# Optimization experiments

Measured on AMD Instinct MI355X. Metric: run time of the kernel, lower is better.

## Reference

```python
import jax, jax.numpy as jnp
import numpy as np
from jax import lax

B, T, D, H = 64, 1024, 256, 512


def setup_inputs() -> dict:
    key = jax.random.key(0)
    k1, k2, k3, k4, k5 = jax.random.split(key, 5)
    s = 1.0 / np.sqrt(H)
    return {
        "x": jax.random.normal(k1, (B, T, D), dtype=jnp.float32),
        "W_ih": jax.random.uniform(k2, (4 * H, D), minval=-s, maxval=s, dtype=jnp.float32),
        "W_hh": jax.random.uniform(k3, (4 * H, H), minval=-s, maxval=s, dtype=jnp.float32),
        "b_ih": jax.random.uniform(k4, (4 * H,), minval=-s, maxval=s, dtype=jnp.float32),
        "b_hh": jax.random.uniform(k5, (4 * H,), minval=-s, maxval=s, dtype=jnp.float32),
    }


def reference(x, W_ih, W_hh, b_ih, b_hh):
    # x: [B, T, D] -> time-major [T, B, D]
    xT = jnp.swapaxes(x, 0, 1)
    b, h_dim = x.shape[0], W_hh.shape[1]
    # Precompute input projections for all timesteps: [T, B, 4H]
    x_proj = jnp.einsum("tbd,gd->tbg", xT, W_ih) + b_ih + b_hh

    def step(carry, xg):
        h, c = carry
        gates = xg + h @ W_hh.T  # [B, 4H]
        i, f, g, o = jnp.split(gates, 4, axis=-1)
        c = jax.nn.sigmoid(f) * c + jax.nn.sigmoid(i) * jnp.tanh(g)
        h = jax.nn.sigmoid(o) * jnp.tanh(c)
        return (h, c), jax.nn.sigmoid(h)

    h0 = jnp.zeros((b, h_dim), dtype=x.dtype)
    c0 = jnp.zeros((b, h_dim), dtype=x.dtype)
    _, outs = lax.scan(step, (h0, c0), x_proj)  # outs: [T, B, H]
    # torch.cat along dim 0 over timesteps -> [T*B, H]
    return outs.reshape(-1, h_dim)
```

## Files before the change

### kernel.cpp

```cpp
#include <hip/hip_runtime.h>
#include <stdint.h>

#define T_STEPS 1024
#define BATCH   64
#define DIN     256
#define HDIM    512
#define G4      2048
#define NGRP    8
#define GWG     32
#define GB      8
#define NBUF    16

#define OFF_XCNT  0
#define OFF_ARR   1024
#define OFF_BIAS  8192
#define OFF_WHH   16384
#define OFF_WIH   (OFF_WHH + G4*HDIM*2)
#define OFF_H     (OFF_WIH + G4*DIN*2)

typedef __attribute__((ext_vector_type(8))) short bf16x8;
typedef __attribute__((ext_vector_type(4))) float f32x4;

__device__ __forceinline__ unsigned short f2bf(float f) {
  union { float f; unsigned u; } v; v.f = f;
  unsigned r = v.u + 0x7FFF + ((v.u >> 16) & 1);
  return (unsigned short)(r >> 16);
}
__device__ __forceinline__ float sigm(float x)   { return 1.0f / (1.0f + __expf(-x)); }
__device__ __forceinline__ float tanh_f(float x) { return 2.0f / (1.0f + __expf(-2.0f * x)) - 1.0f; }

__global__ void k_init(unsigned char* ws) {
  int tid = blockIdx.x * blockDim.x + threadIdx.x;
  unsigned* w32 = (unsigned*)ws;
  for (int i = tid; i < 8192 / 4; i += gridDim.x * blockDim.x) w32[i] = 0;
}

__global__ void k_pack(const float* __restrict__ W_ih, const float* __restrict__ W_hh,
                       const float* __restrict__ b_ih, const float* __restrict__ b_hh,
                       unsigned char* ws) {
  unsigned short* whh = (unsigned short*)(ws + OFF_WHH);
  unsigned short* wih = (unsigned short*)(ws + OFF_WIH);
  float* bias = (float*)(ws + OFF_BIAS);
  int tid = blockIdx.x * blockDim.x + threadIdx.x;
  int np = gridDim.x * blockDim.x;
  for (int i = tid; i < G4 * HDIM; i += np) whh[i] = f2bf(W_hh[i]);
  for (int i = tid; i < G4 * DIN;  i += np) wih[i] = f2bf(W_ih[i]);
  for (int i = tid; i < G4;        i += np) bias[i] = b_ih[i] + b_hh[i];
}

__device__ __forceinline__ void stage_x(const float* __restrict__ x, unsigned short* A_s,
                                        int g, int m, int c, int tstep) {
  const float* xb = x + ((size_t)(g * GB + m) * 1024 + tstep) * 256 + c * 8;
  float4 f0 = *(const float4*)(xb);
  float4 f1 = *(const float4*)(xb + 4);
  union { bf16x8 v; unsigned short s[8]; } u;
  u.s[0] = f2bf(f0.x); u.s[1] = f2bf(f0.y); u.s[2] = f2bf(f0.z); u.s[3] = f2bf(f0.w);
  u.s[4] = f2bf(f1.x); u.s[5] = f2bf(f1.y); u.s[6] = f2bf(f1.z); u.s[7] = f2bf(f1.w);
  *(bf16x8*)(A_s + m * 776 + 512 + c * 8) = u.v;
}

__global__ __launch_bounds__(256, 1) void k_lstm(unsigned char* ws,
                                                 const float* __restrict__ x,
                                                 float* __restrict__ out) {
  __shared__ __attribute__((aligned(16))) unsigned short A_s[16 * 776];
  __shared__ __attribute__((aligned(16))) float glp[4 * 16 * 64];
  __shared__ int s_rank;

  const int tid = threadIdx.x;

  unsigned xcc;
  asm("s_getreg_b32 %0, hwreg(HW_REG_XCC_ID)" : "=s"(xcc));
  xcc &= 7;
  unsigned* xcnt = (unsigned*)(ws + OFF_XCNT);
  if (tid == 0)
    s_rank = (int)__hip_atomic_fetch_add(&xcnt[xcc], 1u, __ATOMIC_RELAXED, __HIP_MEMORY_SCOPE_AGENT);
  __syncthreads();
  const int rank = s_rank;
  if (rank >= GWG) return;

  const int g  = (int)xcc;
  const int jt = rank;

  const unsigned short* whh_g = (const unsigned short*)(ws + OFF_WHH);
  const unsigned short* wih_g = (const unsigned short*)(ws + OFF_WIH);
  const float*          bias_g = (const float*)(ws + OFF_BIAS);
  unsigned short*       hring = (unsigned short*)(ws + OFF_H) + (size_t)g * (NBUF * GB * HDIM);
  unsigned*             arr   = (unsigned*)(ws + OFF_ARR + g * 256);

  const int lane = tid & 63, wave = tid >> 6;
  const int arow = lane & 15;
  const int kg   = (lane >> 4) * 8;
  const int sm   = tid >> 5, sc = tid & 31;

  bf16x8 bq[24];
  {
    #pragma unroll
    for (int u = 0; u < 6; ++u)
      #pragma unroll
      for (int nt = 0; nt < 4; ++nt) {
        int grow = nt * 512 + jt * 16 + (lane & 15);
        const unsigned short* src;
        if (u < 4) src = whh_g + (size_t)grow * 512 + (wave * 4 + u) * 32 + kg;
        else       src = wih_g + (size_t)grow * 256 + (wave * 2 + (u - 4)) * 32 + kg;
        bq[u * 4 + nt] = *(const bf16x8*)src;
      }
  }

  {
    unsigned* a32 = (unsigned*)A_s;
    for (int i = tid; i < 16 * 776 / 2; i += 256) a32[i] = 0;
  }

  float biasr[4];
  float c_reg = 0.f;
  const int ub = tid >> 4, jl = tid & 15;
  if (tid < 128) {
    #pragma unroll
    for (int gt = 0; gt < 4; ++gt)
      biasr[gt] = bias_g[gt * 512 + jt * 16 + jl];
  }

  __syncthreads();

  stage_x(x, A_s, g, sm, sc, 0);
  __syncthreads();
  f32x4 accX[4];
  {
    #pragma unroll
    for (int nt = 0; nt < 4; ++nt) accX[nt] = (f32x4){0.f, 0.f, 0.f, 0.f};
    #pragma unroll
    for (int j = 0; j < 2; ++j) {
      int xk = wave * 2 + j;
      bf16x8 a = *(const bf16x8*)(A_s + arow * 776 + 512 + xk * 32 + kg);
      #pragma unroll
      for (int nt = 0; nt < 4; ++nt)
        accX[nt] = __builtin_amdgcn_mfma_f32_16x16x32_bf16(a, bq[(4 + j) * 4 + nt], accX[nt], 0, 0, 0);
    }
  }
  __syncthreads();
  stage_x(x, A_s, g, sm, sc, 1);
  __syncthreads();

  for (int t = 0; t < T_STEPS; ++t) {
    f32x4 acc[4];
    #pragma unroll
    for (int nt = 0; nt < 4; ++nt) acc[nt] = accX[nt];
    #pragma unroll
    for (int u = 0; u < 4; ++u) {
      int kk = wave * 4 + u;
      bf16x8 a = *(const bf16x8*)(A_s + arow * 776 + kk * 32 + kg);
      #pragma unroll
      for (int nt = 0; nt < 4; ++nt)
        acc[nt] = __builtin_amdgcn_mfma_f32_16x16x32_bf16(a, bq[u * 4 + nt], acc[nt], 0, 0, 0);
    }
    #pragma unroll
    for (int nt = 0; nt < 4; ++nt)
      #pragma unroll
      for (int r = 0; r < 4; ++r) {
        int m = (lane >> 4) * 4 + r;
        glp[wave * 1024 + m * 64 + nt * 16 + (lane & 15)] = acc[nt][r];
      }
    __syncthreads();

    float hv = 0.f;
    if (tid < 128) {
      float gs[4];
      #pragma unroll
      for (int gt = 0; gt < 4; ++gt)
        gs[gt] = glp[ub * 64 + gt * 16 + jl]
               + glp[1024 + ub * 64 + gt * 16 + jl]
               + glp[2048 + ub * 64 + gt * 16 + jl]
               + glp[3072 + ub * 64 + gt * 16 + jl] + biasr[gt];
      float cv = sigm(gs[1]) * c_reg + sigm(gs[0]) * tanh_f(gs[2]);
      c_reg = cv;
      hv = sigm(gs[3]) * tanh_f(cv);
      if (t + 1 < T_STEPS) {
        unsigned short* hd = hring + (size_t)((t + 1) & (NBUF - 1)) * (GB * HDIM);
        hd[ub * HDIM + jt * 16 + jl] = f2bf(hv);
        asm volatile("s_waitcnt vmcnt(0)" ::: "memory");
        if (lane == 0)
          __hip_atomic_fetch_add(&arr[wave * 32], 1u,
                                 __ATOMIC_RELAXED, __HIP_MEMORY_SCOPE_WORKGROUP);
      }
      out[((size_t)t * 64 + g * GB + ub) * 512 + jt * 16 + jl] = sigm(hv);
    }

    if (t + 1 < T_STEPS) {
      #pragma unroll
      for (int nt = 0; nt < 4; ++nt) accX[nt] = (f32x4){0.f, 0.f, 0.f, 0.f};
      #pragma unroll
      for (int j = 0; j < 2; ++j) {
        int xk = wave * 2 + j;
        bf16x8 a = *(const bf16x8*)(A_s + arow * 776 + 512 + xk * 32 + kg);
        #pragma unroll
        for (int nt = 0; nt < 4; ++nt)
          accX[nt] = __builtin_amdgcn_mfma_f32_16x16x32_bf16(a, bq[(4 + j) * 4 + nt], accX[nt], 0, 0, 0);
      }
      if (tid == 192) {
        const unsigned target = 32u * (unsigned)(t + 1);
        for (;;) {
          unsigned v0 = __hip_atomic_fetch_or(&arr[0], 0x80000000u,
                                              __ATOMIC_RELAXED, __HIP_MEMORY_SCOPE_WORKGROUP);
          unsigned v1 = __hip_atomic_fetch_or(&arr[32], 0x80000000u,
                                              __ATOMIC_RELAXED, __HIP_MEMORY_SCOPE_WORKGROUP);
          if ((v0 & 0x7FFFFFFFu) >= target && (v1 & 0x7FFFFFFFu) >= target) break;
        }
      }
      __syncthreads();
      {
        const unsigned short* hs = hring + (size_t)((t + 1) & (NBUF - 1)) * (GB * HDIM)
                                 + sm * HDIM + sc * 16;
        bf16x8 h0 = *(const bf16x8*)(hs);
        bf16x8 h1 = *(const bf16x8*)(hs + 8);
        *(bf16x8*)(A_s + sm * 776 + sc * 16)     = h0;
        *(bf16x8*)(A_s + sm * 776 + sc * 16 + 8) = h1;
        if (t + 2 < T_STEPS) stage_x(x, A_s, g, sm, sc, t + 2);
      }
      __syncthreads();
    }
  }
}

extern "C" void kernel_launch(void* const* d_in, const int* in_sizes, int n_in,
                              void* d_out, int out_size, void* d_ws, size_t ws_size,
                              hipStream_t stream) {
  const float* x    = (const float*)d_in[0];
  const float* W_ih = (const float*)d_in[1];
  const float* W_hh = (const float*)d_in[2];
  const float* b_ih = (const float*)d_in[3];
  const float* b_hh = (const float*)d_in[4];
  float* out = (float*)d_out;
  unsigned char* ws = (unsigned char*)d_ws;

  hipLaunchKernelGGL(k_init, dim3(8),    dim3(256), 0, stream, ws);
  hipLaunchKernelGGL(k_pack, dim3(1024), dim3(256), 0, stream, W_ih, W_hh, b_ih, b_hh, ws);
  hipLaunchKernelGGL(k_lstm, dim3(512),  dim3(256), 0, stream, ws, x, out);
}
```

Baseline: 2.849 ms.

## Double workgroup to 8 waves, split gate columns per wave, stage weights in LDS

Workgroups grow from 4 to 8 waves. Each wave now owns one 16-column gate tile, and the K dimension is split unevenly: four waves cover the last four h-chunks plus the whole x projection, the other four cover the first twelve h-chunks. Weights move from per-lane registers into LDS, and the cross-wave reduction shrinks from four partials to two. The arrival counter becomes a single word polled with s_sleep. The intent is shorter per-step MFMA chains on the serial critical path, paid for with LDS reads of the weights every step and a larger block.

```diff
diff --git a/kernel.cpp b/kernel.cpp
--- a/kernel.cpp
+++ b/kernel.cpp
@@ -10,6 +10,7 @@
 #define GWG     32
 #define GB      8
 #define NBUF    16
+#define BLOCK   512
 
 #define OFF_XCNT  0
 #define OFF_ARR   1024
@@ -59,11 +60,13 @@
   *(bf16x8*)(A_s + m * 776 + 512 + c * 8) = u.v;
 }
 
-__global__ __launch_bounds__(256, 1) void k_lstm(unsigned char* ws,
-                                                 const float* __restrict__ x,
-                                                 float* __restrict__ out) {
+__global__ __launch_bounds__(BLOCK, 1) void k_lstm(unsigned char* ws,
+                                                   const float* __restrict__ x,
+                                                   float* __restrict__ out) {
   __shared__ __attribute__((aligned(16))) unsigned short A_s[16 * 776];
-  __shared__ __attribute__((aligned(16))) float glp[4 * 16 * 64];
+  __shared__ __attribute__((aligned(16))) unsigned short Whh_s[64 * 520];
+  __shared__ __attribute__((aligned(16))) unsigned short Wih_s[64 * 264];
+  __shared__ __attribute__((aligned(16))) float glp[2 * 16 * 64];
   __shared__ int s_rank;
 
   const int tid = threadIdx.x;
@@ -85,30 +88,31 @@
   const unsigned short* wih_g = (const unsigned short*)(ws + OFF_WIH);
   const float*          bias_g = (const float*)(ws + OFF_BIAS);
   unsigned short*       hring = (unsigned short*)(ws + OFF_H) + (size_t)g * (NBUF * GB * HDIM);
-  unsigned*             arr   = (unsigned*)(ws + OFF_ARR + g * 256);
-
-  const int lane = tid & 63, wave = tid >> 6;
+  unsigned*             arr   = (unsigned*)(ws + OFF_ARR + g * 128);
+
+  const int lane = tid & 63, w = tid >> 6;
+  const int ns   = w & 3;
+  const int whigh = (w < 4);
   const int arow = lane & 15;
   const int kg   = (lane >> 4) * 8;
-  const int sm   = tid >> 5, sc = tid & 31;
-
-  bf16x8 bq[24];
+  const int rl   = ns * 16 + (lane & 15);
+
   {
-    #pragma unroll
-    for (int u = 0; u < 6; ++u)
-      #pragma unroll
-      for (int nt = 0; nt < 4; ++nt) {
-        int grow = nt * 512 + jt * 16 + (lane & 15);
-        const unsigned short* src;
-        if (u < 4) src = whh_g + (size_t)grow * 512 + (wave * 4 + u) * 32 + kg;
-        else       src = wih_g + (size_t)grow * 256 + (wave * 2 + (u - 4)) * 32 + kg;
-        bq[u * 4 + nt] = *(const bf16x8*)src;
-      }
+    int rl0 = tid >> 3, part = tid & 7;
+    int grow = (rl0 >> 4) * 512 + jt * 16 + (rl0 & 15);
+    const unsigned short* src = whh_g + (size_t)grow * 512 + part * 64;
+    unsigned short* dst = Whh_s + rl0 * 520 + part * 64;
+    #pragma unroll
+    for (int i = 0; i < 8; ++i) *(bf16x8*)(dst + i * 8) = *(const bf16x8*)(src + i * 8);
+    const unsigned short* src2 = wih_g + (size_t)grow * 256 + part * 32;
+    unsigned short* dst2 = Wih_s + rl0 * 264 + part * 32;
+    #pragma unroll
+    for (int i = 0; i < 4; ++i) *(bf16x8*)(dst2 + i * 8) = *(const bf16x8*)(src2 + i * 8);
   }
 
   {
     unsigned* a32 = (unsigned*)A_s;
-    for (int i = tid; i < 16 * 776 / 2; i += 256) a32[i] = 0;
+    for (int i = tid; i < 16 * 776 / 2; i += BLOCK) a32[i] = 0;
   }
 
   float biasr[4];
@@ -120,46 +124,71 @@
       biasr[gt] = bias_g[gt * 512 + jt * 16 + jl];
   }
 
-  __syncthreads();
-
-  stage_x(x, A_s, g, sm, sc, 0);
-  __syncthreads();
-  f32x4 accX[4];
-  {
-    #pragma unroll
-    for (int nt = 0; nt < 4; ++nt) accX[nt] = (f32x4){0.f, 0.f, 0.f, 0.f};
-    #pragma unroll
-    for (int j = 0; j < 2; ++j) {
-      int xk = wave * 2 + j;
+  const int sm = tid >> 6, sc = tid & 63;
+
+  __syncthreads();
+
+  if (sc < 32) stage_x(x, A_s, g, sm, sc, 0);
+  __syncthreads();
+  f32x4 accX = {0.f, 0.f, 0.f, 0.f};
+  if (whigh) {
+    f32x4 xa = {0.f,0.f,0.f,0.f}, xb2 = {0.f,0.f,0.f,0.f};
+    #pragma unroll
+    for (int xk = 0; xk < 4; ++xk) {
       bf16x8 a = *(const bf16x8*)(A_s + arow * 776 + 512 + xk * 32 + kg);
-      #pragma unroll
-      for (int nt = 0; nt < 4; ++nt)
-        accX[nt] = __builtin_amdgcn_mfma_f32_16x16x32_bf16(a, bq[(4 + j) * 4 + nt], accX[nt], 0, 0, 0);
-    }
-  }
-  __syncthreads();
-  stage_x(x, A_s, g, sm, sc, 1);
+      bf16x8 b = *(const bf16x8*)(Wih_s + rl * 264 + xk * 32 + kg);
+      xa = __builtin_amdgcn_mfma_f32_16x16x32_bf16(a, b, xa, 0, 0, 0);
+    }
+    #pragma unroll
+    for (int xk = 4; xk < 8; ++xk) {
+      bf16x8 a = *(const bf16x8*)(A_s + arow * 776 + 512 + xk * 32 + kg);
+      bf16x8 b = *(const bf16x8*)(Wih_s + rl * 264 + xk * 32 + kg);
+      xb2 = __builtin_amdgcn_mfma_f32_16x16x32_bf16(a, b, xb2, 0, 0, 0);
+    }
+    #pragma unroll
+    for (int r = 0; r < 4; ++r) accX[r] = xa[r] + xb2[r];
+  }
+  __syncthreads();
+  if (sc < 32) stage_x(x, A_s, g, sm, sc, 1);
   __syncthreads();
 
   for (int t = 0; t < T_STEPS; ++t) {
-    f32x4 acc[4];
-    #pragma unroll
-    for (int nt = 0; nt < 4; ++nt) acc[nt] = accX[nt];
-    #pragma unroll
-    for (int u = 0; u < 4; ++u) {
-      int kk = wave * 4 + u;
-      bf16x8 a = *(const bf16x8*)(A_s + arow * 776 + kk * 32 + kg);
-      #pragma unroll
-      for (int nt = 0; nt < 4; ++nt)
-        acc[nt] = __builtin_amdgcn_mfma_f32_16x16x32_bf16(a, bq[u * 4 + nt], acc[nt], 0, 0, 0);
-    }
-    #pragma unroll
-    for (int nt = 0; nt < 4; ++nt)
+    f32x4 accfin;
+    if (whigh) {
+      f32x4 a0 = accX;
+      #pragma unroll
+      for (int u = 0; u < 4; ++u) {
+        int kk = 12 + u;
+        bf16x8 a = *(const bf16x8*)(A_s + arow * 776 + kk * 32 + kg);
+        bf16x8 b = *(const bf16x8*)(Whh_s + rl * 520 + kk * 32 + kg);
+        a0 = __builtin_amdgcn_mfma_f32_16x16x32_bf16(a, b, a0, 0, 0, 0);
+      }
+      accfin = a0;
+    } else {
+      f32x4 a0 = {0.f,0.f,0.f,0.f}, a1 = {0.f,0.f,0.f,0.f};
+      #pragma unroll
+      for (int u = 0; u < 6; ++u) {
+        bf16x8 a = *(const bf16x8*)(A_s + arow * 776 + u * 32 + kg);
+        bf16x8 b = *(const bf16x8*)(Whh_s + rl * 520 + u * 32 + kg);
+        a0 = __builtin_amdgcn_mfma_f32_16x16x32_bf16(a, b, a0, 0, 0, 0);
+      }
+      #pragma unroll
+      for (int u = 6; u < 12; ++u) {
+        bf16x8 a = *(const bf16x8*)(A_s + arow * 776 + u * 32 + kg);
+        bf16x8 b = *(const bf16x8*)(Whh_s + rl * 520 + u * 32 + kg);
+        a1 = __builtin_amdgcn_mfma_f32_16x16x32_bf16(a, b, a1, 0, 0, 0);
+      }
+      #pragma unroll
+      for (int r = 0; r < 4; ++r) accfin[r] = a0[r] + a1[r];
+    }
+    {
+      const int half = whigh ? 1 : 0;
       #pragma unroll
       for (int r = 0; r < 4; ++r) {
         int m = (lane >> 4) * 4 + r;
-        glp[wave * 1024 + m * 64 + nt * 16 + (lane & 15)] = acc[nt][r];
-      }
+        glp[half * 1024 + m * 64 + ns * 16 + (lane & 15)] = accfin[r];
+      }
+    }
     __syncthreads();
 
     float hv = 0.f;
@@ -168,53 +197,60 @@
       #pragma unroll
       for (int gt = 0; gt < 4; ++gt)
         gs[gt] = glp[ub * 64 + gt * 16 + jl]
-               + glp[1024 + ub * 64 + gt * 16 + jl]
-               + glp[2048 + ub * 64 + gt * 16 + jl]
-               + glp[3072 + ub * 64 + gt * 16 + jl] + biasr[gt];
+               + glp[1024 + ub * 64 + gt * 16 + jl] + biasr[gt];
       float cv = sigm(gs[1]) * c_reg + sigm(gs[0]) * tanh_f(gs[2]);
       c_reg = cv;
       hv = sigm(gs[3]) * tanh_f(cv);
       if (t + 1 < T_STEPS) {
         unsigned short* hd = hring + (size_t)((t + 1) & (NBUF - 1)) * (GB * HDIM);
         hd[ub * HDIM + jt * 16 + jl] = f2bf(hv);
+      }
+    }
+
+    if (t + 1 < T_STEPS) {
+      if (whigh) {
+        f32x4 xa = {0.f,0.f,0.f,0.f}, xb2 = {0.f,0.f,0.f,0.f};
+        #pragma unroll
+        for (int xk = 0; xk < 4; ++xk) {
+          bf16x8 a = *(const bf16x8*)(A_s + arow * 776 + 512 + xk * 32 + kg);
+          bf16x8 b = *(const bf16x8*)(Wih_s + rl * 264 + xk * 32 + kg);
+          xa = __builtin_amdgcn_mfma_f32_16x16x32_bf16(a, b, xa, 0, 0, 0);
+        }
+        #pragma unroll
+        for (int xk = 4; xk < 8; ++xk) {
+          bf16x8 a = *(const bf16x8*)(A_s + arow * 776 + 512 + xk * 32 + kg);
+          bf16x8 b = *(const bf16x8*)(Wih_s + rl * 264 + xk * 32 + kg);
+          xb2 = __builtin_amdgcn_mfma_f32_16x16x32_bf16(a, b, xb2, 0, 0, 0);
+        }
+        #pragma unroll
+        for (int r = 0; r < 4; ++r) accX[r] = xa[r] + xb2[r];
+      }
+      if (tid < 128) {
         asm volatile("s_waitcnt vmcnt(0)" ::: "memory");
         if (lane == 0)
-          __hip_atomic_fetch_add(&arr[wave * 32], 1u,
-                                 __ATOMIC_RELAXED, __HIP_MEMORY_SCOPE_WORKGROUP);
-      }
+          __hip_atomic_fetch_add(arr, 1u, __ATOMIC_RELAXED, __HIP_MEMORY_SCOPE_WORKGROUP);
+      }
+    }
+    if (tid < 128)
       out[((size_t)t * 64 + g * GB + ub) * 512 + jt * 16 + jl] = sigm(hv);
-    }
 
     if (t + 1 < T_STEPS) {
-      #pragma unroll
-      for (int nt = 0; nt < 4; ++nt) accX[nt] = (f32x4){0.f, 0.f, 0.f, 0.f};
-      #pragma unroll
-      for (int j = 0; j < 2; ++j) {
-        int xk = wave * 2 + j;
-        bf16x8 a = *(const bf16x8*)(A_s + arow * 776 + 512 + xk * 32 + kg);
-        #pragma unroll
-        for (int nt = 0; nt < 4; ++nt)
-          accX[nt] = __builtin_amdgcn_mfma_f32_16x16x32_bf16(a, bq[(4 + j) * 4 + nt], accX[nt], 0, 0, 0);
-      }
-      if (tid == 192) {
-        const unsigned target = 32u * (unsigned)(t + 1);
+      if (tid == 256) {
+        const unsigned target = 64u * (unsigned)(t + 1);
         for (;;) {
-          unsigned v0 = __hip_atomic_fetch_or(&arr[0], 0x80000000u,
-                                              __ATOMIC_RELAXED, __HIP_MEMORY_SCOPE_WORKGROUP);
-          unsigned v1 = __hip_atomic_fetch_or(&arr[32], 0x80000000u,
-                                              __ATOMIC_RELAXED, __HIP_MEMORY_SCOPE_WORKGROUP);
-          if ((v0 & 0x7FFFFFFFu) >= target && (v1 & 0x7FFFFFFFu) >= target) break;
+          unsigned v = __hip_atomic_fetch_or(arr, 0x80000000u,
+                                             __ATOMIC_RELAXED, __HIP_MEMORY_SCOPE_WORKGROUP);
+          if ((v & 0x7FFFFFFFu) >= target) break;
+          __builtin_amdgcn_s_sleep(2);
         }
       }
       __syncthreads();
       {
         const unsigned short* hs = hring + (size_t)((t + 1) & (NBUF - 1)) * (GB * HDIM)
-                                 + sm * HDIM + sc * 16;
+                                 + sm * HDIM + sc * 8;
         bf16x8 h0 = *(const bf16x8*)(hs);
-        bf16x8 h1 = *(const bf16x8*)(hs + 8);
-        *(bf16x8*)(A_s + sm * 776 + sc * 16)     = h0;
-        *(bf16x8*)(A_s + sm * 776 + sc * 16 + 8) = h1;
-        if (t + 2 < T_STEPS) stage_x(x, A_s, g, sm, sc, t + 2);
+        *(bf16x8*)(A_s + sm * 776 + sc * 8) = h0;
+        if (t + 2 < T_STEPS && sc < 32) stage_x(x, A_s, g, sm, sc, t + 2);
       }
       __syncthreads();
     }
@@ -234,5 +270,5 @@
 
   hipLaunchKernelGGL(k_init, dim3(8),    dim3(256), 0, stream, ws);
   hipLaunchKernelGGL(k_pack, dim3(1024), dim3(256), 0, stream, W_ih, W_hh, b_ih, b_hh, ws);
-  hipLaunchKernelGGL(k_lstm, dim3(512),  dim3(256), 0, stream, ws, x, out);
-}
+  hipLaunchKernelGGL(k_lstm, dim3(512),  dim3(BLOCK), 0, stream, ws, x, out);
+}
```

Result: slower. 3.271 ms (+14.8%).
